# Kernel optimization log

Hardware: AMD Instinct MI355X
Metric: run time of the kernel (lower is better)

The kernel has to match this reference:

```python
import jax, jax.numpy as jnp
import numpy as np

N = 12288          # total active voxels
B = 4              # batch (scans)
D = 128            # latent_dim
TAU = 0.1          # heat threshold
RADIUS = 1.1       # peak-suppression radius (loop=True => self included)
R_CLUSTER = 1.1    # cluster radius (undefined in source; set = RADIUS)


def setup_inputs() -> dict:
    key = jax.random.key(0)
    k1, k2, k3 = jax.random.split(key, 3)
    feats = jax.random.normal(k1, (N, D), jnp.float32)
    spatial = jax.random.randint(k2, (N, 3), 0, 64).astype(jnp.int32)
    batch = (jnp.arange(N) // (N // B)).astype(jnp.int32)
    coords = jnp.concatenate([batch[:, None], spatial], axis=1)  # [N,4] (b,x,y,z)
    # 1x1 Conv3d == Linear; kaiming_normal fan_out (fan_out = 1) -> std = sqrt(2)
    W = jax.random.normal(k3, (D, 1), jnp.float32) * jnp.sqrt(2.0)
    p = 0.01  # instance_density
    b = jnp.full((1,), np.log(p / (1.0 - p)), jnp.float32)
    return {"feats": feats, "W": W, "b": b, "coords": coords}


def reference(feats, W, b, coords):
    # 1x1 sparse conv = per-point linear projection
    logits = feats @ W + b                    # [N,1] centroid scores
    heat = jax.nn.sigmoid(logits[:, 0])       # [N]
    valid = heat > TAU                        # candidate mask (fixed-shape analog of boolean indexing)

    pos = coords[:, 1:].astype(jnp.float32)   # [N,3]
    bidx = coords[:, 0]                       # [N]
    # pairwise squared distances via gram trick (avoids [N,N,3] intermediate)
    sq = jnp.sum(pos * pos, axis=-1)
    d2 = sq[:, None] + sq[None, :] - 2.0 * (pos @ pos.T)   # [N,N]
    same_b = bidx[:, None] == bidx[None, :]

    # radius_graph(cand, r=RADIUS, loop=True): i<-j edges among valid candidates
    within = same_b & (d2 <= RADIUS * RADIUS) & valid[:, None] & valid[None, :]
    # scatter_max of neighbor heats onto each candidate
    neigh_max = jnp.max(jnp.where(within, heat[None, :], -jnp.inf), axis=1)
    is_peak = valid & (heat >= neigh_max)

    # peak -> candidate cluster edges within R_CLUSTER; scatter_mean of candidate feats
    within_c = same_b & (d2 <= R_CLUSTER * R_CLUSTER) & valid[None, :] & is_peak[:, None]
    w = within_c.astype(feats.dtype)                      # [N,N]
    cnt = jnp.maximum(jnp.sum(w, axis=1, keepdims=True), 1.0)
    feat_mean = (w @ feats) / cnt                         # [N,D], nonzero rows only at peaks

    peaks = jnp.where(is_peak[:, None], coords, 0)        # [N,4], zeroed non-peak rows
    return logits, peaks, feat_mean
```

## Files before the change

### kernel.cpp

```cpp
#include <hip/hip_runtime.h>
#include <cmath>

#define NPTS 12288
#define NB   4
#define MB   3072
#define DF   128
#define TAUF 0.1f
#define NI   24
#define INVALID_PK 0x00FFFFFFu

static __device__ __forceinline__ unsigned sad_u8(unsigned a, unsigned b) {
#if __has_builtin(__builtin_amdgcn_sad_u8)
    return __builtin_amdgcn_sad_u8(a, b, 0u);
#else
    unsigned d, z = 0u;
    asm("v_sad_u8 %0, %1, %2, %3" : "=v"(d) : "v"(a), "v"(b), "v"(z));
    return d;
#endif
}

__global__ __launch_bounds__(256) void k_logits(
    const float* __restrict__ feats, const float* __restrict__ W,
    const float* __restrict__ bias, const int* __restrict__ coords,
    float* __restrict__ out_logits, unsigned* __restrict__ pts_pk,
    float* __restrict__ pts_h)
{
    const int gtid = blockIdx.x * 256 + threadIdx.x;
    const int row  = gtid >> 6;
    const int lane = gtid & 63;
    const float2 f = ((const float2*)(feats + (size_t)row * DF))[lane];
    const float2 w = ((const float2*)W)[lane];
    float s = f.x * w.x + f.y * w.y;
    #pragma unroll
    for (int off = 32; off; off >>= 1) s += __shfl_xor(s, off);
    if (lane == 0) {
        const float logit = s + bias[0];
        out_logits[row] = logit;
        const float heat = 1.0f / (1.0f + expf(-logit));
        const bool valid = heat > TAUF;
        const int4 c = ((const int4*)coords)[row];
        pts_pk[row] = valid ? ((unsigned)c.y | ((unsigned)c.z << 8) | ((unsigned)c.w << 16))
                            : INVALID_PK;
        pts_h[row]  = valid ? heat : -INFINITY;
    }
}

__global__ __launch_bounds__(256) void k_main(
    const float* __restrict__ feats, const unsigned* __restrict__ pts_pk,
    const float* __restrict__ pts_h,
    float* __restrict__ out_peaks, float* __restrict__ out_mean)
{
    __shared__ unsigned s_pk[MB];
    __shared__ float    s_h[MB];
    const int tid   = threadIdx.x;
    const int iBase = blockIdx.x * NI;
    const int batch = iBase / MB;
    const int bBase = batch * MB;
    {
        uint4* d1 = (uint4*)s_pk;  const uint4* g1 = (const uint4*)(pts_pk + bBase);
        uint4* d2 = (uint4*)s_h;   const uint4* g2 = (const uint4*)(pts_h  + bBase);
        #pragma unroll
        for (int k = 0; k < MB / 4 / 256; ++k) {
            d1[tid + k * 256] = g1[tid + k * 256];
            d2[tid + k * 256] = g2[tid + k * 256];
        }
    }
    __syncthreads();

    const int wave = tid >> 6, lane = tid & 63;
    const int i0 = iBase + wave * 6;

    unsigned pip[6];
    float    ph[6];
    unsigned mmlo[6], mmhi[6];
    #pragma unroll
    for (int q = 0; q < 6; ++q) {
        pip[q] = s_pk[i0 - bBase + q];
        ph[q]  = s_h[i0 - bBase + q];
        mmlo[q] = 0u; mmhi[q] = 0u;
    }

    #pragma unroll
    for (int t = 0; t < 32; ++t) {
        const unsigned pj = s_pk[t * 64 + lane];
        #pragma unroll
        for (int q = 0; q < 6; ++q) {
            const bool cc = sad_u8(pip[q], pj) <= 1u;
            mmlo[q] |= cc ? (1u << t) : 0u;
        }
    }
    #pragma unroll
    for (int t = 32; t < 48; ++t) {
        const unsigned pj = s_pk[t * 64 + lane];
        #pragma unroll
        for (int q = 0; q < 6; ++q) {
            const bool cc = sad_u8(pip[q], pj) <= 1u;
            mmhi[q] |= cc ? (1u << (t - 32)) : 0u;
        }
    }

    #pragma unroll
    for (int q = 0; q < 6; ++q) {
        const int i = i0 + q;
        const unsigned long long mm = (unsigned long long)mmlo[q]
                                    | ((unsigned long long)mmhi[q] << 32);
        const bool validi = (pip[q] != INVALID_PK);
        float nm = -INFINITY;
        int   cnt = 0;
        if (validi) {
            unsigned long long bal = __ballot(mm != 0ull);
            while (bal) {
                const int sl = __builtin_ctzll(bal);
                bal &= bal - 1;
                unsigned long long m2 = __shfl(mm, sl);
                cnt += __popcll(m2);
                while (m2) {
                    const int t = __builtin_ctzll(m2);
                    m2 &= m2 - 1;
                    nm = fmaxf(nm, s_h[t * 64 + sl]);
                }
            }
        }
        const bool is_peak = validi && (ph[q] >= nm);

        if (lane == 0) {
            const float4 pk = is_peak
                ? make_float4((float)batch, (float)(pip[q] & 255u),
                              (float)((pip[q] >> 8) & 255u), (float)(pip[q] >> 16))
                : make_float4(0.f, 0.f, 0.f, 0.f);
            ((float4*)out_peaks)[i] = pk;
        }

        float* om = out_mean + (size_t)i * DF;
        if (is_peak) {
            float a0 = 0.f, a1 = 0.f;
            unsigned long long bal = __ballot(mm != 0ull);
            while (bal) {
                const int sl = __builtin_ctzll(bal);
                bal &= bal - 1;
                unsigned long long m2 = __shfl(mm, sl);
                while (m2) {
                    const int t = __builtin_ctzll(m2);
                    m2 &= m2 - 1;
                    const float* fj = feats + (size_t)(bBase + t * 64 + sl) * DF;
                    a0 += fj[lane];
                    a1 += fj[64 + lane];
                }
            }
            const float fc = (float)cnt;
            om[lane]      = a0 / fc;
            om[64 + lane] = a1 / fc;
        } else {
            om[lane]      = 0.f;
            om[64 + lane] = 0.f;
        }
    }
}

extern "C" void kernel_launch(void* const* d_in, const int* in_sizes, int n_in,
                              void* d_out, int out_size, void* d_ws, size_t ws_size,
                              hipStream_t stream) {
    const float* feats  = (const float*)d_in[0];
    const float* W      = (const float*)d_in[1];
    const float* bias   = (const float*)d_in[2];
    const int*   coords = (const int*)d_in[3];

    float* out        = (float*)d_out;
    float* out_logits = out;
    float* out_peaks  = out + NPTS;
    float* out_mean   = out + NPTS * 5;

    unsigned* pts_pk = (unsigned*)d_ws;
    float*    pts_h  = (float*)((char*)d_ws + 65536);

    k_logits<<<NPTS / 4, 256, 0, stream>>>(feats, W, bias, coords,
                                           out_logits, pts_pk, pts_h);
    k_main<<<NPTS / NI, 256, 0, stream>>>(feats, pts_pk, pts_h,
                                          out_peaks, out_mean);
}
```

Baseline: 19.37 us.

## Replace brute-force per-batch neighbor scan with voxel hash grid linked lists

Builds a dense cell-head table over the 4×64³ voxel grid with atomicExch-linked lists in the logits kernel. The main kernel now looks up only the 7 face-adjacent cells per point instead of comparing against all 3072 points in the batch. This removes the O(N·MB) SAD comparison work and the shared-memory staging. In exchange it adds a 4 MB head-clear kernel and a third launch, plus serialized pointer-chasing through global memory.

Measured after the change: 20.19 us. 4.2% more time.

```diff
diff --git a/kernel.cpp b/kernel.cpp
--- a/kernel.cpp
+++ b/kernel.cpp
@@ -2,28 +2,22 @@
 #include <cmath>
 
 #define NPTS 12288
-#define NB   4
-#define MB   3072
 #define DF   128
 #define TAUF 0.1f
-#define NI   24
-#define INVALID_PK 0x00FFFFFFu
+#define CELL_BITS 18
+#define NCELLS (4 << CELL_BITS)
+#define INVALID_PK 0xFFFFFFFFu
 
-static __device__ __forceinline__ unsigned sad_u8(unsigned a, unsigned b) {
-#if __has_builtin(__builtin_amdgcn_sad_u8)
-    return __builtin_amdgcn_sad_u8(a, b, 0u);
-#else
-    unsigned d, z = 0u;
-    asm("v_sad_u8 %0, %1, %2, %3" : "=v"(d) : "v"(a), "v"(b), "v"(z));
-    return d;
-#endif
+__global__ __launch_bounds__(256) void k_fill(int4* __restrict__ head4)
+{
+    head4[blockIdx.x * 256 + threadIdx.x] = make_int4(-1, -1, -1, -1);
 }
 
 __global__ __launch_bounds__(256) void k_logits(
     const float* __restrict__ feats, const float* __restrict__ W,
     const float* __restrict__ bias, const int* __restrict__ coords,
     float* __restrict__ out_logits, unsigned* __restrict__ pts_pk,
-    float* __restrict__ pts_h)
+    float* __restrict__ pts_h, int* __restrict__ head, int* __restrict__ nxt)
 {
     const int gtid = blockIdx.x * 256 + threadIdx.x;
     const int row  = gtid >> 6;
@@ -39,122 +33,80 @@
         const float heat = 1.0f / (1.0f + expf(-logit));
         const bool valid = heat > TAUF;
         const int4 c = ((const int4*)coords)[row];
-        pts_pk[row] = valid ? ((unsigned)c.y | ((unsigned)c.z << 8) | ((unsigned)c.w << 16))
+        pts_pk[row] = valid ? ((unsigned)c.y | ((unsigned)c.z << 8) |
+                               ((unsigned)c.w << 16) | ((unsigned)c.x << 24))
                             : INVALID_PK;
         pts_h[row]  = valid ? heat : -INFINITY;
+        if (valid) {
+            const int cell = (c.x << CELL_BITS) | c.y | (c.z << 6) | (c.w << 12);
+            nxt[row] = atomicExch(head + cell, row);
+        }
     }
 }
 
 __global__ __launch_bounds__(256) void k_main(
-    const float* __restrict__ feats, const unsigned* __restrict__ pts_pk,
-    const float* __restrict__ pts_h,
+    const float* __restrict__ feats, const int* __restrict__ head,
+    const unsigned* __restrict__ pts_pk, const float* __restrict__ pts_h,
+    const int* __restrict__ nxt,
     float* __restrict__ out_peaks, float* __restrict__ out_mean)
 {
-    __shared__ unsigned s_pk[MB];
-    __shared__ float    s_h[MB];
-    const int tid   = threadIdx.x;
-    const int iBase = blockIdx.x * NI;
-    const int batch = iBase / MB;
-    const int bBase = batch * MB;
-    {
-        uint4* d1 = (uint4*)s_pk;  const uint4* g1 = (const uint4*)(pts_pk + bBase);
-        uint4* d2 = (uint4*)s_h;   const uint4* g2 = (const uint4*)(pts_h  + bBase);
-        #pragma unroll
-        for (int k = 0; k < MB / 4 / 256; ++k) {
-            d1[tid + k * 256] = g1[tid + k * 256];
-            d2[tid + k * 256] = g2[tid + k * 256];
-        }
-    }
-    __syncthreads();
+    const int wave = threadIdx.x >> 6;
+    const int lane = threadIdx.x & 63;
+    const int i    = blockIdx.x * 4 + wave;
 
-    const int wave = tid >> 6, lane = tid & 63;
-    const int i0 = iBase + wave * 6;
+    const unsigned pk = pts_pk[i];
+    float2* om = (float2*)(out_mean + (size_t)i * DF);
 
-    unsigned pip[6];
-    float    ph[6];
-    unsigned mmlo[6], mmhi[6];
-    #pragma unroll
-    for (int q = 0; q < 6; ++q) {
-        pip[q] = s_pk[i0 - bBase + q];
-        ph[q]  = s_h[i0 - bBase + q];
-        mmlo[q] = 0u; mmhi[q] = 0u;
+    if (pk == INVALID_PK) {
+        if (lane == 0) ((float4*)out_peaks)[i] = make_float4(0.f, 0.f, 0.f, 0.f);
+        om[lane] = make_float2(0.f, 0.f);
+        return;
     }
 
-    #pragma unroll
-    for (int t = 0; t < 32; ++t) {
-        const unsigned pj = s_pk[t * 64 + lane];
-        #pragma unroll
-        for (int q = 0; q < 6; ++q) {
-            const bool cc = sad_u8(pip[q], pj) <= 1u;
-            mmlo[q] |= cc ? (1u << t) : 0u;
-        }
-    }
-    #pragma unroll
-    for (int t = 32; t < 48; ++t) {
-        const unsigned pj = s_pk[t * 64 + lane];
-        #pragma unroll
-        for (int q = 0; q < 6; ++q) {
-            const bool cc = sad_u8(pip[q], pj) <= 1u;
-            mmhi[q] |= cc ? (1u << (t - 32)) : 0u;
-        }
+    const int x = pk & 255u, y = (pk >> 8) & 255u, z = (pk >> 16) & 255u, b = pk >> 24;
+    const float hi = pts_h[i];
+
+    int j = -1;
+    if (lane < 7) {
+        const int nx = x + ((lane == 1) - (lane == 2));
+        const int ny = y + ((lane == 3) - (lane == 4));
+        const int nz = z + ((lane == 5) - (lane == 6));
+        if (((unsigned)nx < 64u) && ((unsigned)ny < 64u) && ((unsigned)nz < 64u))
+            j = head[(b << CELL_BITS) | nx | (ny << 6) | (nz << 12)];
     }
 
+    float nm = -INFINITY;
+    int   cnt = 0;
+    for (int t = j; t >= 0; t = nxt[t]) { nm = fmaxf(nm, pts_h[t]); ++cnt; }
     #pragma unroll
-    for (int q = 0; q < 6; ++q) {
-        const int i = i0 + q;
-        const unsigned long long mm = (unsigned long long)mmlo[q]
-                                    | ((unsigned long long)mmhi[q] << 32);
-        const bool validi = (pip[q] != INVALID_PK);
-        float nm = -INFINITY;
-        int   cnt = 0;
-        if (validi) {
-            unsigned long long bal = __ballot(mm != 0ull);
-            while (bal) {
-                const int sl = __builtin_ctzll(bal);
-                bal &= bal - 1;
-                unsigned long long m2 = __shfl(mm, sl);
-                cnt += __popcll(m2);
-                while (m2) {
-                    const int t = __builtin_ctzll(m2);
-                    m2 &= m2 - 1;
-                    nm = fmaxf(nm, s_h[t * 64 + sl]);
-                }
-            }
-        }
-        const bool is_peak = validi && (ph[q] >= nm);
+    for (int off = 1; off < 8; off <<= 1) {
+        nm   = fmaxf(nm, __shfl_xor(nm, off));
+        cnt += __shfl_xor(cnt, off);
+    }
+    nm  = __shfl(nm, 0);
+    cnt = __shfl(cnt, 0);
 
-        if (lane == 0) {
-            const float4 pk = is_peak
-                ? make_float4((float)batch, (float)(pip[q] & 255u),
-                              (float)((pip[q] >> 8) & 255u), (float)(pip[q] >> 16))
-                : make_float4(0.f, 0.f, 0.f, 0.f);
-            ((float4*)out_peaks)[i] = pk;
-        }
+    const bool is_peak = (hi >= nm);
+    if (lane == 0) {
+        ((float4*)out_peaks)[i] = is_peak
+            ? make_float4((float)b, (float)x, (float)y, (float)z)
+            : make_float4(0.f, 0.f, 0.f, 0.f);
+    }
+    if (!is_peak) { om[lane] = make_float2(0.f, 0.f); return; }
 
-        float* om = out_mean + (size_t)i * DF;
-        if (is_peak) {
-            float a0 = 0.f, a1 = 0.f;
-            unsigned long long bal = __ballot(mm != 0ull);
-            while (bal) {
-                const int sl = __builtin_ctzll(bal);
-                bal &= bal - 1;
-                unsigned long long m2 = __shfl(mm, sl);
-                while (m2) {
-                    const int t = __builtin_ctzll(m2);
-                    m2 &= m2 - 1;
-                    const float* fj = feats + (size_t)(bBase + t * 64 + sl) * DF;
-                    a0 += fj[lane];
-                    a1 += fj[64 + lane];
-                }
-            }
-            const float fc = (float)cnt;
-            om[lane]      = a0 / fc;
-            om[64 + lane] = a1 / fc;
-        } else {
-            om[lane]      = 0.f;
-            om[64 + lane] = 0.f;
-        }
+    float2 a = make_float2(0.f, 0.f);
+    int cur = j;
+    for (;;) {
+        const unsigned long long bal = __ballot(cur >= 0);
+        if (!bal) break;
+        const int sl = __builtin_ctzll(bal);
+        const int jj = __shfl(cur, sl);
+        const float2 fv = ((const float2*)(feats + (size_t)jj * DF))[lane];
+        a.x += fv.x; a.y += fv.y;
+        if (lane == sl) cur = nxt[cur];
     }
+    const float fc = (float)cnt;
+    om[lane] = make_float2(a.x / fc, a.y / fc);
 }
 
 extern "C" void kernel_launch(void* const* d_in, const int* in_sizes, int n_in,
@@ -170,11 +122,14 @@
     float* out_peaks  = out + NPTS;
     float* out_mean   = out + NPTS * 5;
 
-    unsigned* pts_pk = (unsigned*)d_ws;
-    float*    pts_h  = (float*)((char*)d_ws + 65536);
+    int*      head   = (int*)d_ws;
+    unsigned* pts_pk = (unsigned*)((char*)d_ws + (4u << 20));
+    float*    pts_h  = (float*)((char*)d_ws + (4u << 20) + 65536);
+    int*      nxt    = (int*)((char*)d_ws + (4u << 20) + 131072);
 
-    k_logits<<<NPTS / 4, 256, 0, stream>>>(feats, W, bias, coords,
-                                           out_logits, pts_pk, pts_h);
-    k_main<<<NPTS / NI, 256, 0, stream>>>(feats, pts_pk, pts_h,
-                                          out_peaks, out_mean);
+    k_fill  <<<NCELLS / 4 / 256, 256, 0, stream>>>((int4*)head);
+    k_logits<<<NPTS / 4,         256, 0, stream>>>(feats, W, bias, coords,
+                                                   out_logits, pts_pk, pts_h, head, nxt);
+    k_main  <<<NPTS / 4,         256, 0, stream>>>(feats, head, pts_pk, pts_h, nxt,
+                                                   out_peaks, out_mean);
 }
```

## Fuse logits and peak kernels into one cooperative launch with grid sync

Applied to the files above, without the earlier changes.

Merges the logit/heat kernel and the main peak/cluster kernel into a single cooperative kernel. Each wave computes logits for its own six rows, publishes them to the workspace, then a grid-wide barrier precedes the shared-memory staging and neighbour search. This removes one kernel launch and the inter-kernel gap, at the cost of a grid sync and the need for all 512 blocks to be co-resident.

Measured after the change: 69.07 us. +256.6%, slower.

```diff
diff --git a/kernel.cpp b/kernel.cpp
--- a/kernel.cpp
+++ b/kernel.cpp
@@ -1,4 +1,5 @@
 #include <hip/hip_runtime.h>
+#include <hip/hip_cooperative_groups.h>
 #include <cmath>
 
 #define NPTS 12288
@@ -19,43 +20,50 @@
 #endif
 }
 
-__global__ __launch_bounds__(256) void k_logits(
+__global__ __launch_bounds__(256) void k_fused(
     const float* __restrict__ feats, const float* __restrict__ W,
     const float* __restrict__ bias, const int* __restrict__ coords,
-    float* __restrict__ out_logits, unsigned* __restrict__ pts_pk,
-    float* __restrict__ pts_h)
-{
-    const int gtid = blockIdx.x * 256 + threadIdx.x;
-    const int row  = gtid >> 6;
-    const int lane = gtid & 63;
-    const float2 f = ((const float2*)(feats + (size_t)row * DF))[lane];
-    const float2 w = ((const float2*)W)[lane];
-    float s = f.x * w.x + f.y * w.y;
-    #pragma unroll
-    for (int off = 32; off; off >>= 1) s += __shfl_xor(s, off);
-    if (lane == 0) {
-        const float logit = s + bias[0];
-        out_logits[row] = logit;
-        const float heat = 1.0f / (1.0f + expf(-logit));
-        const bool valid = heat > TAUF;
-        const int4 c = ((const int4*)coords)[row];
-        pts_pk[row] = valid ? ((unsigned)c.y | ((unsigned)c.z << 8) | ((unsigned)c.w << 16))
-                            : INVALID_PK;
-        pts_h[row]  = valid ? heat : -INFINITY;
-    }
-}
-
-__global__ __launch_bounds__(256) void k_main(
-    const float* __restrict__ feats, const unsigned* __restrict__ pts_pk,
-    const float* __restrict__ pts_h,
-    float* __restrict__ out_peaks, float* __restrict__ out_mean)
+    float* __restrict__ out_logits, float* __restrict__ out_peaks,
+    float* __restrict__ out_mean,
+    unsigned* __restrict__ pts_pk, float* __restrict__ pts_h)
 {
     __shared__ unsigned s_pk[MB];
     __shared__ float    s_h[MB];
     const int tid   = threadIdx.x;
+    const int wave  = tid >> 6, lane = tid & 63;
     const int iBase = blockIdx.x * NI;
     const int batch = iBase / MB;
     const int bBase = batch * MB;
+    const int i0    = iBase + wave * 6;
+
+    const float2 w2 = ((const float2*)W)[lane];
+    const float  bv = bias[0];
+
+    unsigned pip[6];
+    float    ph[6];
+    #pragma unroll
+    for (int q = 0; q < 6; ++q) {
+        const int row = i0 + q;
+        const float2 f = ((const float2*)(feats + (size_t)row * DF))[lane];
+        float s = f.x * w2.x + f.y * w2.y;
+        #pragma unroll
+        for (int off = 32; off; off >>= 1) s += __shfl_xor(s, off);
+        const float logit = s + bv;
+        const float heat  = 1.0f / (1.0f + expf(-logit));
+        const bool  valid = heat > TAUF;
+        const int4  c = ((const int4*)coords)[row];
+        pip[q] = valid ? ((unsigned)c.y | ((unsigned)c.z << 8) | ((unsigned)c.w << 16))
+                       : INVALID_PK;
+        ph[q]  = valid ? heat : -INFINITY;
+        if (lane == 0) {
+            out_logits[row] = logit;
+            pts_pk[row] = pip[q];
+            pts_h[row]  = ph[q];
+        }
+    }
+
+    cooperative_groups::this_grid().sync();
+
     {
         uint4* d1 = (uint4*)s_pk;  const uint4* g1 = (const uint4*)(pts_pk + bBase);
         uint4* d2 = (uint4*)s_h;   const uint4* g2 = (const uint4*)(pts_h  + bBase);
@@ -67,18 +75,9 @@
     }
     __syncthreads();
 
-    const int wave = tid >> 6, lane = tid & 63;
-    const int i0 = iBase + wave * 6;
-
-    unsigned pip[6];
-    float    ph[6];
     unsigned mmlo[6], mmhi[6];
     #pragma unroll
-    for (int q = 0; q < 6; ++q) {
-        pip[q] = s_pk[i0 - bBase + q];
-        ph[q]  = s_h[i0 - bBase + q];
-        mmlo[q] = 0u; mmhi[q] = 0u;
-    }
+    for (int q = 0; q < 6; ++q) { mmlo[q] = 0u; mmhi[q] = 0u; }
 
     #pragma unroll
     for (int t = 0; t < 32; ++t) {
@@ -173,8 +172,9 @@
     unsigned* pts_pk = (unsigned*)d_ws;
     float*    pts_h  = (float*)((char*)d_ws + 65536);
 
-    k_logits<<<NPTS / 4, 256, 0, stream>>>(feats, W, bias, coords,
-                                           out_logits, pts_pk, pts_h);
-    k_main<<<NPTS / NI, 256, 0, stream>>>(feats, pts_pk, pts_h,
-                                          out_peaks, out_mean);
+    void* args[] = { (void*)&feats, (void*)&W, (void*)&bias, (void*)&coords,
+                     (void*)&out_logits, (void*)&out_peaks, (void*)&out_mean,
+                     (void*)&pts_pk, (void*)&pts_h };
+    hipLaunchCooperativeKernel((const void*)k_fused, dim3(NPTS / NI), dim3(256),
+                               args, 0, stream);
 }
```
